# Optimization experiments

Hardware: AMD Instinct MI355X
Metric: run time of the kernel (lower is better)

The kernel has to match this reference:

```python
import jax, jax.numpy as jnp
import numpy as np

EPS = 1e-6

def _feature(x):
    # phi(x) = concat(relu(x), relu(-x)) along the last dim: (b,h,n,d) -> (b,h,n,2d)
    return jnp.concatenate([jax.nn.relu(x), jax.nn.relu(-x)], axis=-1)

def setup_inputs() -> dict:
    key = jax.random.key(0)
    kq, kk, kv = jax.random.split(key, 3)
    shape = (4, 16, 8192, 64)  # (batch, heads, seq_len, dim)
    Q = jax.random.normal(kq, shape, dtype=jnp.float32)
    K = jax.random.normal(kk, shape, dtype=jnp.float32)
    V = jax.random.normal(kv, shape, dtype=jnp.float32)
    return {"Q": Q, "K": K, "V": V}

def reference(Q, K, V):
    Qf = _feature(Q)  # (b,h,n,2d)
    Kf = _feature(K)  # (b,h,n,2d)
    # KV outer-product reduction over sequence: (b,h,2d,m)
    KV = jnp.einsum('bhnd,bhnm->bhdm', Kf, V)
    out = jnp.einsum('bhnd,bhdm->bhnm', Qf, KV)  # (b,h,n,m)
    K_sum = Kf.sum(axis=2)  # (b,h,2d)
    normalizer = jnp.einsum('bhnd,bhd->bhn', Qf, K_sum)  # (b,h,n)
    return out / (normalizer[..., None] + EPS)
```

## Files before the change

kernel.cpp:

```cpp
#include <hip/hip_runtime.h>

typedef __bf16 bf16x8 __attribute__((ext_vector_type(8)));
typedef __bf16 bf16x4 __attribute__((ext_vector_type(4)));
typedef float f32x4 __attribute__((ext_vector_type(4)));

#define BH_TOT 64
#define SEQ 8192
#define DIM 64
#define NCH 16
#define CHN (SEQ / NCH)
#define KV_STRIDE 68
#define KV_ROWS 128

__global__ __launch_bounds__(256) void fla_ph1(const float* __restrict__ K,
                                               const float* __restrict__ V,
                                               float* __restrict__ kvf) {
  const int blk = blockIdx.x;
  const int bh = blk / NCH;
  const int ch = blk % NCH;
  const float* Kp = K + (size_t)bh * SEQ * DIM + (size_t)ch * CHN * DIM;
  const float* Vp = V + (size_t)bh * SEQ * DIM + (size_t)ch * CHN * DIM;

  __shared__ __bf16 Kb[32][68];
  __shared__ __bf16 Vb[32][68];

  const int tid = threadIdx.x;
  const int lane = tid & 63;
  const int w = tid >> 6;
  const int quad = lane >> 4;
  const int col = lane & 15;

  f32x4 acc[2][5];
#pragma unroll
  for (int mt = 0; mt < 2; ++mt)
#pragma unroll
    for (int nt = 0; nt < 5; ++nt)
      acc[mt][nt] = (f32x4){0.f, 0.f, 0.f, 0.f};

  bf16x8 bones;
#pragma unroll
  for (int j = 0; j < 8; ++j) bones[j] = (__bf16)0.f;
  if (col == 0) {
#pragma unroll
    for (int j = 0; j < 8; ++j) bones[j] = (__bf16)1.0f;
  }

  const int fcol0 = ((w & 1) << 5) + col;
  const bool neg = (w >= 2);

  for (int s = 0; s < CHN / 32; ++s) {
    const float* Ks = Kp + s * 32 * DIM;
    const float* Vs = Vp + s * 32 * DIM;
    __syncthreads();
#pragma unroll
    for (int i = 0; i < 2; ++i) {
      int idx = tid + i * 256;
      int r = idx >> 4;
      int c4 = (idx & 15) << 2;
      float4 kk = *(const float4*)(Ks + r * DIM + c4);
      float4 vv = *(const float4*)(Vs + r * DIM + c4);
      bf16x4 kb4, vb4;
      kb4[0] = (__bf16)kk.x; kb4[1] = (__bf16)kk.y;
      kb4[2] = (__bf16)kk.z; kb4[3] = (__bf16)kk.w;
      vb4[0] = (__bf16)vv.x; vb4[1] = (__bf16)vv.y;
      vb4[2] = (__bf16)vv.z; vb4[3] = (__bf16)vv.w;
      *(bf16x4*)&Kb[r][c4] = kb4;
      *(bf16x4*)&Vb[r][c4] = vb4;
    }
    __syncthreads();

    bf16x8 a0, a1, bfr[5];
#pragma unroll
    for (int j = 0; j < 8; ++j) {
      int rr = quad * 8 + j;
      float k0 = (float)Kb[rr][fcol0];
      float k1 = (float)Kb[rr][fcol0 + 16];
      if (neg) { k0 = -k0; k1 = -k1; }
      a0[j] = (__bf16)fmaxf(k0, 0.f);
      a1[j] = (__bf16)fmaxf(k1, 0.f);
      bfr[0][j] = Vb[rr][col];
      bfr[1][j] = Vb[rr][col + 16];
      bfr[2][j] = Vb[rr][col + 32];
      bfr[3][j] = Vb[rr][col + 48];
    }
    bfr[4] = bones;
#pragma unroll
    for (int nt = 0; nt < 5; ++nt) {
      acc[0][nt] = __builtin_amdgcn_mfma_f32_16x16x32_bf16(a0, bfr[nt], acc[0][nt], 0, 0, 0);
      acc[1][nt] = __builtin_amdgcn_mfma_f32_16x16x32_bf16(a1, bfr[nt], acc[1][nt], 0, 0, 0);
    }
  }

  float* dst = kvf + (size_t)bh * KV_ROWS * KV_STRIDE;
#pragma unroll
  for (int mt = 0; mt < 2; ++mt) {
    int feat = (w * 2 + mt) * 16 + quad * 4;
#pragma unroll
    for (int nt = 0; nt < 5; ++nt) {
      int c = nt * 16 + col;
      if (c <= 64) {
#pragma unroll
        for (int r = 0; r < 4; ++r)
          atomicAdd(&dst[(size_t)(feat + r) * KV_STRIDE + c], acc[mt][nt][r]);
      }
    }
  }
}

__global__ __launch_bounds__(256) void fla_ph2(const float* __restrict__ Q,
                                               const float* __restrict__ kvf,
                                               float* __restrict__ out) {
  const int blk = blockIdx.x;
  const int bh = blk >> 5;
  const int rb = blk & 31;
  const float* Qp = Q + (size_t)bh * SEQ * DIM + (size_t)rb * 256 * DIM;
  float* Op = out + (size_t)bh * SEQ * DIM + (size_t)rb * 256 * DIM;

  __shared__ __bf16 kvb[128][66];
  const float* src = kvf + (size_t)bh * KV_ROWS * KV_STRIDE;
  for (int i = threadIdx.x; i < 128 * 66; i += 256) {
    int k = i / 66;
    int c = i - k * 66;
    float v = (c <= 64) ? src[(size_t)k * KV_STRIDE + c] : 0.f;
    kvb[k][c] = (__bf16)v;
  }
  __syncthreads();

  const int lane = threadIdx.x & 63;
  const int w = threadIdx.x >> 6;
  const int quad = lane >> 4;
  const int col = lane & 15;

  bf16x8 bfr[4][5];
#pragma unroll
  for (int kt = 0; kt < 4; ++kt) {
#pragma unroll
    for (int j = 0; j < 8; ++j) {
      int k = kt * 32 + quad * 8 + j;
      bfr[kt][0][j] = kvb[k][col];
      bfr[kt][1][j] = kvb[k][col + 16];
      bfr[kt][2][j] = kvb[k][col + 32];
      bfr[kt][3][j] = kvb[k][col + 48];
      bfr[kt][4][j] = (col == 0) ? kvb[k][64] : (__bf16)0.f;
    }
  }

#pragma unroll
  for (int mt = 0; mt < 4; ++mt) {
    const float* qrow = Qp + (size_t)(w * 64 + mt * 16 + col) * DIM;
    float4 q0 = *(const float4*)(qrow + quad * 8);
    float4 q1 = *(const float4*)(qrow + quad * 8 + 4);
    float4 q2 = *(const float4*)(qrow + 32 + quad * 8);
    float4 q3 = *(const float4*)(qrow + 32 + quad * 8 + 4);
    float qv[16];
    *(float4*)&qv[0] = q0;  *(float4*)&qv[4] = q1;
    *(float4*)&qv[8] = q2;  *(float4*)&qv[12] = q3;
    bf16x8 a0, a1, a2, a3;
#pragma unroll
    for (int j = 0; j < 8; ++j) {
      a0[j] = (__bf16)fmaxf(qv[j], 0.f);
      a2[j] = (__bf16)fmaxf(-qv[j], 0.f);
      a1[j] = (__bf16)fmaxf(qv[8 + j], 0.f);
      a3[j] = (__bf16)fmaxf(-qv[8 + j], 0.f);
    }
    f32x4 acc[5];
#pragma unroll
    for (int nt = 0; nt < 5; ++nt) acc[nt] = (f32x4){0.f, 0.f, 0.f, 0.f};
#pragma unroll
    for (int nt = 0; nt < 5; ++nt) {
      acc[nt] = __builtin_amdgcn_mfma_f32_16x16x32_bf16(a0, bfr[0][nt], acc[nt], 0, 0, 0);
      acc[nt] = __builtin_amdgcn_mfma_f32_16x16x32_bf16(a1, bfr[1][nt], acc[nt], 0, 0, 0);
      acc[nt] = __builtin_amdgcn_mfma_f32_16x16x32_bf16(a2, bfr[2][nt], acc[nt], 0, 0, 0);
      acc[nt] = __builtin_amdgcn_mfma_f32_16x16x32_bf16(a3, bfr[3][nt], acc[nt], 0, 0, 0);
    }
    float inv[4];
#pragma unroll
    for (int r = 0; r < 4; ++r) {
      float nrm = __shfl((float)acc[4][r], lane & 48, 64);
      inv[r] = 1.0f / (nrm + 1e-6f);
    }
    float* orow = Op + (size_t)(w * 64 + mt * 16) * DIM;
#pragma unroll
    for (int nt = 0; nt < 4; ++nt)
#pragma unroll
      for (int r = 0; r < 4; ++r)
        orow[(size_t)(quad * 4 + r) * DIM + nt * 16 + col] = acc[nt][r] * inv[r];
  }
}

extern "C" void kernel_launch(void* const* d_in, const int* in_sizes, int n_in,
                              void* d_out, int out_size, void* d_ws, size_t ws_size,
                              hipStream_t stream) {
  const float* Q = (const float*)d_in[0];
  const float* K = (const float*)d_in[1];
  const float* V = (const float*)d_in[2];
  float* out = (float*)d_out;
  float* kvf = (float*)d_ws;

  hipMemsetAsync(kvf, 0, (size_t)BH_TOT * KV_ROWS * KV_STRIDE * sizeof(float), stream);
  fla_ph1<<<dim3(BH_TOT * NCH), dim3(256), 0, stream>>>(K, V, kvf);
  fla_ph2<<<dim3(BH_TOT * 32), dim3(256), 0, stream>>>(Q, kvf, out);
}
```

Measured before the change: 472.4 us.

## Load K/V fragments directly from global memory, drop LDS staging and syncs

```diff
diff --git a/kernel.cpp b/kernel.cpp
--- a/kernel.cpp
+++ b/kernel.cpp
@@ -1,28 +1,24 @@
 #include <hip/hip_runtime.h>
 
 typedef __bf16 bf16x8 __attribute__((ext_vector_type(8)));
-typedef __bf16 bf16x4 __attribute__((ext_vector_type(4)));
 typedef float f32x4 __attribute__((ext_vector_type(4)));
 
 #define BH_TOT 64
 #define SEQ 8192
 #define DIM 64
-#define NCH 16
+#define NCH 32
 #define CHN (SEQ / NCH)
 #define KV_STRIDE 68
 #define KV_ROWS 128
 
-__global__ __launch_bounds__(256) void fla_ph1(const float* __restrict__ K,
-                                               const float* __restrict__ V,
-                                               float* __restrict__ kvf) {
+__global__ __launch_bounds__(256, 4) void fla_ph1(const float* __restrict__ K,
+                                                  const float* __restrict__ V,
+                                                  float* __restrict__ kvf) {
   const int blk = blockIdx.x;
   const int bh = blk / NCH;
   const int ch = blk % NCH;
   const float* Kp = K + (size_t)bh * SEQ * DIM + (size_t)ch * CHN * DIM;
   const float* Vp = V + (size_t)bh * SEQ * DIM + (size_t)ch * CHN * DIM;
-
-  __shared__ __bf16 Kb[32][68];
-  __shared__ __bf16 Vb[32][68];
 
   const int tid = threadIdx.x;
   const int lane = tid & 63;
@@ -46,42 +42,30 @@
   }
 
   const int fcol0 = ((w & 1) << 5) + col;
-  const bool neg = (w >= 2);
+  const float sgn = (w >= 2) ? -1.0f : 1.0f;
 
   for (int s = 0; s < CHN / 32; ++s) {
-    const float* Ks = Kp + s * 32 * DIM;
-    const float* Vs = Vp + s * 32 * DIM;
-    __syncthreads();
+    const float* Kr = Kp + (size_t)(s * 32 + quad * 8) * DIM;
+    const float* Vr = Vp + (size_t)(s * 32 + quad * 8) * DIM;
+    float k0[8], k1[8], v0[8], v1[8], v2[8], v3[8];
 #pragma unroll
-    for (int i = 0; i < 2; ++i) {
-      int idx = tid + i * 256;
-      int r = idx >> 4;
-      int c4 = (idx & 15) << 2;
-      float4 kk = *(const float4*)(Ks + r * DIM + c4);
-      float4 vv = *(const float4*)(Vs + r * DIM + c4);
-      bf16x4 kb4, vb4;
-      kb4[0] = (__bf16)kk.x; kb4[1] = (__bf16)kk.y;
-      kb4[2] = (__bf16)kk.z; kb4[3] = (__bf16)kk.w;
-      vb4[0] = (__bf16)vv.x; vb4[1] = (__bf16)vv.y;
-      vb4[2] = (__bf16)vv.z; vb4[3] = (__bf16)vv.w;
-      *(bf16x4*)&Kb[r][c4] = kb4;
-      *(bf16x4*)&Vb[r][c4] = vb4;
+    for (int j = 0; j < 8; ++j) {
+      k0[j] = Kr[j * DIM + fcol0];
+      k1[j] = Kr[j * DIM + fcol0 + 16];
+      v0[j] = Vr[j * DIM + col];
+      v1[j] = Vr[j * DIM + col + 16];
+      v2[j] = Vr[j * DIM + col + 32];
+      v3[j] = Vr[j * DIM + col + 48];
     }
-    __syncthreads();
-
     bf16x8 a0, a1, bfr[5];
 #pragma unroll
     for (int j = 0; j < 8; ++j) {
-      int rr = quad * 8 + j;
-      float k0 = (float)Kb[rr][fcol0];
-      float k1 = (float)Kb[rr][fcol0 + 16];
-      if (neg) { k0 = -k0; k1 = -k1; }
-      a0[j] = (__bf16)fmaxf(k0, 0.f);
-      a1[j] = (__bf16)fmaxf(k1, 0.f);
-      bfr[0][j] = Vb[rr][col];
-      bfr[1][j] = Vb[rr][col + 16];
-      bfr[2][j] = Vb[rr][col + 32];
-      bfr[3][j] = Vb[rr][col + 48];
+      a0[j] = (__bf16)fmaxf(sgn * k0[j], 0.f);
+      a1[j] = (__bf16)fmaxf(sgn * k1[j], 0.f);
+      bfr[0][j] = (__bf16)v0[j];
+      bfr[1][j] = (__bf16)v1[j];
+      bfr[2][j] = (__bf16)v2[j];
+      bfr[3][j] = (__bf16)v3[j];
     }
     bfr[4] = bones;
 #pragma unroll
@@ -107,9 +91,9 @@
   }
 }
 
-__global__ __launch_bounds__(256) void fla_ph2(const float* __restrict__ Q,
-                                               const float* __restrict__ kvf,
-                                               float* __restrict__ out) {
+__global__ __launch_bounds__(256, 4) void fla_ph2(const float* __restrict__ Q,
+                                                  const float* __restrict__ kvf,
+                                                  float* __restrict__ out) {
   const int blk = blockIdx.x;
   const int bh = blk >> 5;
   const int rb = blk & 31;
```

Measured after the change: 566.2 us. 19.9% more time.
